# Kernel optimization log

Hardware: AMD Instinct MI355X
Metric: run time of the kernel (lower is better)

The kernel has to match this reference:

```python
import jax, jax.numpy as jnp
import numpy as np

N_NODES = 100000
IN_CH, HID_CH, OUT_CH = 128, 256, 128
N_EDGES = 1600000


def setup_inputs() -> dict:
    key = jax.random.key(0)
    k_x, k_e, k_w1, k_b1, k_w2, k_b2 = jax.random.split(key, 6)
    x = jax.random.normal(k_x, (N_NODES, IN_CH), dtype=jnp.float32)
    edge_index = jax.random.randint(k_e, (2, N_EDGES), 0, N_NODES, dtype=jnp.int64)
    # MLP params (Linear stores weight [out,in]; we keep [in,out] for x @ W)
    lim1 = 1.0 / np.sqrt(IN_CH)
    lim2 = 1.0 / np.sqrt(HID_CH)
    W1 = jax.random.uniform(k_w1, (IN_CH, HID_CH), jnp.float32, -lim1, lim1)
    b1 = jax.random.uniform(k_b1, (HID_CH,), jnp.float32, -lim1, lim1)
    W2 = jax.random.uniform(k_w2, (HID_CH, OUT_CH), jnp.float32, -lim2, lim2)
    b2 = jax.random.uniform(k_b2, (OUT_CH,), jnp.float32, -lim2, lim2)
    eps = jnp.zeros((), jnp.float32)  # train_eps=True, init 0
    return {"x": x, "edge_index": edge_index, "W1": W1, "b1": b1,
            "W2": W2, "b2": b2, "eps": eps}


def reference(x, edge_index, W1, b1, W2, b2, eps):
    src, dst = edge_index[0], edge_index[1]
    # scatter-add neighbor aggregation: aggr[i] = sum_{(j->i)} x[j]
    aggr = jax.ops.segment_sum(x[src], dst, num_segments=N_NODES)  # [N, in]
    h = (1.0 + eps) * x + aggr
    h = jax.nn.relu(h @ W1 + b1)
    h = h @ W2 + b2
    h = jax.nn.relu(h)
    # dropout is identity in eval mode
    return jax.nn.log_softmax(h, axis=-1)
```

## Files before the change

### kernel.cpp

```cpp
#include <hip/hip_runtime.h>

#define N_NODES 100000
#define IN_CH 128
#define HID_CH 256
#define OUT_CH 128
#define N_EDGES 1600000

#define NBK 782
#define BIN_BLOCKS 256
#define EPB (N_EDGES / BIN_BLOCKS)
#define BKT_CAP 4096

typedef __attribute__((ext_vector_type(8))) short short8;
typedef __attribute__((ext_vector_type(4))) float f32x4;

__device__ __forceinline__ float b2f(ushort u) {
    unsigned int x = ((unsigned int)u) << 16;
    return __uint_as_float(x);
}
__device__ __forceinline__ ushort f2b(float f) {
    unsigned int u = __float_as_uint(f);
    u += 0x7FFFu + ((u >> 16) & 1u);
    return (ushort)(u >> 16);
}

#define PREP_X_BLOCKS 6250
#define PREP_W1_BLOCKS 128
#define PREP_W2_BLOCKS 128
#define PREP_TOTAL (PREP_X_BLOCKS + PREP_W1_BLOCKS + PREP_W2_BLOCKS)
__global__ __launch_bounds__(256) void prep_kernel(
    const float* __restrict__ x, const float* __restrict__ W1,
    const float* __restrict__ W2, const int* __restrict__ dst,
    ushort* __restrict__ xb, ushort* __restrict__ W1T,
    ushort* __restrict__ W2T, int* __restrict__ histT) {
    const int b = blockIdx.x;
    const int t = threadIdx.x;
    if (b < PREP_X_BLOCKS) {
        const size_t i = (size_t)b * 2048 + t * 8;
        float4 a = *reinterpret_cast<const float4*>(x + i);
        float4 c = *reinterpret_cast<const float4*>(x + i + 4);
        ushort v[8] = {f2b(a.x), f2b(a.y), f2b(a.z), f2b(a.w),
                       f2b(c.x), f2b(c.y), f2b(c.z), f2b(c.w)};
        *reinterpret_cast<short8*>(xb + i) = *reinterpret_cast<short8*>(v);
    } else if (b < PREP_X_BLOCKS + PREP_W1_BLOCKS) {
        const int i = (b - PREP_X_BLOCKS) * 256 + t;
        const int oc = i >> 7, k = i & 127;
        W1T[i] = f2b(W1[k * HID_CH + oc]);
    } else if (b < PREP_TOTAL) {
        const int i = (b - PREP_X_BLOCKS - PREP_W1_BLOCKS) * 256 + t;
        const int oc = i >> 8, k = i & 255;
        W2T[i] = f2b(W2[k * OUT_CH + oc]);
    } else {
        __shared__ int h[NBK];
        const int bb = b - PREP_TOTAL;
        for (int k = t; k < NBK; k += 256) h[k] = 0;
        __syncthreads();
        const int base = bb * EPB;
        for (int i = t; i < EPB; i += 256)
            atomicAdd(&h[dst[base + i] >> 7], 1);
        __syncthreads();
        for (int k = t; k < NBK; k += 256) histT[k * BIN_BLOCKS + bb] = h[k];
    }
}

__global__ __launch_bounds__(256) void scanA_kernel(
    const int* __restrict__ histT, int* __restrict__ blockBaseP,
    int* __restrict__ bktTotal) {
    __shared__ int ts[256];
    const int bk = blockIdx.x, t = threadIdx.x;
    const int v = histT[bk * BIN_BLOCKS + t];
    ts[t] = v;
    __syncthreads();
    #pragma unroll
    for (int o = 1; o < 256; o <<= 1) {
        int add = (t >= o) ? ts[t - o] : 0;
        __syncthreads();
        ts[t] += add;
        __syncthreads();
    }
    blockBaseP[bk * BIN_BLOCKS + t] = ts[t] - v;
    if (t == 255) bktTotal[bk] = ts[255];
}

__global__ __launch_bounds__(256) void bin_kernel(
    const int* __restrict__ src, const int* __restrict__ dst,
    const int* __restrict__ blockBaseP,
    unsigned int* __restrict__ ebuf) {
    __shared__ int base[NBK];
    __shared__ int cur[NBK];
    const int b = blockIdx.x, t = threadIdx.x;
    for (int k = t; k < NBK; k += 256) {
        base[k] = k * BKT_CAP + blockBaseP[k * BIN_BLOCKS + b];
        cur[k] = 0;
    }
    __syncthreads();
    const int ebase = b * EPB;
    for (int i = t; i < EPB; i += 256) {
        const int d = dst[ebase + i];
        const int s = src[ebase + i];
        const int bk = d >> 7;
        const int r = atomicAdd(&cur[bk], 1);
        ebuf[base[bk] + r] = ((unsigned int)(d & 127) << 17) | (unsigned int)s;
    }
}

__global__ __launch_bounds__(256) void group_kernel(
    const unsigned int* __restrict__ ebuf,
    const int* __restrict__ bktTotal,
    int* __restrict__ csr_src, int* __restrict__ begA, int* __restrict__ endA) {
    __shared__ int hist[128];
    __shared__ int cur[128];
    const int bk = blockIdx.x, t = threadIdx.x;
    if (t < 128) hist[t] = 0;
    __syncthreads();
    const int start = bk * BKT_CAP;
    const int cnt   = bktTotal[bk];
    for (int i = t; i < cnt; i += 256)
        atomicAdd(&hist[ebuf[start + i] >> 17], 1);
    __syncthreads();
    int v = (t < 128) ? hist[t] : 0;
    #pragma unroll
    for (int o = 1; o < 128; o <<= 1) {
        int add = (t < 128 && t >= o) ? hist[t - o] : 0;
        __syncthreads();
        if (t < 128) hist[t] += add;
        __syncthreads();
    }
    if (t < 128) {
        const int excl = hist[t] - v;
        cur[t] = excl;
        const int node = bk * 128 + t;
        if (node < N_NODES) {
            begA[node] = start + excl;
            endA[node] = start + hist[t];
        }
    }
    __syncthreads();
    for (int i = t; i < cnt; i += 256) {
        const unsigned int e = ebuf[start + i];
        const int dl = e >> 17;
        const int p = atomicAdd(&cur[dl], 1);
        csr_src[start + p] = (int)(e & 0x1FFFF);
    }
}

__global__ __launch_bounds__(256) void gather_kernel(
    const ushort* __restrict__ xb,
    const float* __restrict__ eps_p,
    const int* __restrict__ begA,
    const int* __restrict__ endA,
    const int* __restrict__ csr_src,
    ushort* __restrict__ h_in) {
    const int node = blockIdx.x * 8 + (threadIdx.x >> 5);
    const int l32 = threadIdx.x & 31;
    const int c = l32 * 4;
    const int beg = begA[node];
    const int end = endA[node];

    float4 A0 = {0.f,0.f,0.f,0.f}, A1 = {0.f,0.f,0.f,0.f};
    float4 A2 = {0.f,0.f,0.f,0.f}, A3 = {0.f,0.f,0.f,0.f};

    for (int base = beg; base < end; base += 32) {
        const int nn = min(32, end - base);
        const int sidx = csr_src[base + min(l32, nn - 1)];
        int i = 0;
        for (; i + 4 <= nn; i += 4) {
            const int s0 = __shfl(sidx, i + 0, 32);
            const int s1 = __shfl(sidx, i + 1, 32);
            const int s2 = __shfl(sidx, i + 2, 32);
            const int s3 = __shfl(sidx, i + 3, 32);
            ushort4 v0 = *reinterpret_cast<const ushort4*>(xb + (size_t)s0 * IN_CH + c);
            ushort4 v1 = *reinterpret_cast<const ushort4*>(xb + (size_t)s1 * IN_CH + c);
            ushort4 v2 = *reinterpret_cast<const ushort4*>(xb + (size_t)s2 * IN_CH + c);
            ushort4 v3 = *reinterpret_cast<const ushort4*>(xb + (size_t)s3 * IN_CH + c);
            A0.x += b2f(v0.x); A0.y += b2f(v0.y); A0.z += b2f(v0.z); A0.w += b2f(v0.w);
            A1.x += b2f(v1.x); A1.y += b2f(v1.y); A1.z += b2f(v1.z); A1.w += b2f(v1.w);
            A2.x += b2f(v2.x); A2.y += b2f(v2.y); A2.z += b2f(v2.z); A2.w += b2f(v2.w);
            A3.x += b2f(v3.x); A3.y += b2f(v3.y); A3.z += b2f(v3.z); A3.w += b2f(v3.w);
        }
        for (; i < nn; ++i) {
            const int s = __shfl(sidx, i, 32);
            ushort4 v = *reinterpret_cast<const ushort4*>(xb + (size_t)s * IN_CH + c);
            A0.x += b2f(v.x); A0.y += b2f(v.y); A0.z += b2f(v.z); A0.w += b2f(v.w);
        }
    }

    const float a0 = A0.x + A1.x + A2.x + A3.x;
    const float a1 = A0.y + A1.y + A2.y + A3.y;
    const float a2 = A0.z + A1.z + A2.z + A3.z;
    const float a3 = A0.w + A1.w + A2.w + A3.w;

    const float scale = 1.0f + eps_p[0];
    ushort4 sv = *reinterpret_cast<const ushort4*>(xb + (size_t)node * IN_CH + c);
    ushort4 o;
    o.x = f2b(scale * b2f(sv.x) + a0);
    o.y = f2b(scale * b2f(sv.y) + a1);
    o.z = f2b(scale * b2f(sv.z) + a2);
    o.w = f2b(scale * b2f(sv.w) + a3);
    *reinterpret_cast<ushort4*>(h_in + (size_t)node * IN_CH + c) = o;
}

__global__ __launch_bounds__(512, 4) void mlp_fused(
    const ushort* __restrict__ h_in,
    const ushort* __restrict__ W1T,
    const ushort* __restrict__ W2T,
    const float* __restrict__ b1,
    const float* __restrict__ b2,
    float* __restrict__ out) {
    __shared__ ushort wbuf[32768];
    const int t    = threadIdx.x;
    const int w    = t >> 6;
    const int lane = t & 63;
    const int lr   = lane & 15;
    const int lk   = lane >> 4;
    const int row0 = blockIdx.x * 128 + w * 16;
    const int arow = row0 + lr;
    const int arc  = arow < N_NODES ? arow : N_NODES - 1;
    const int sw = (lr & 7) << 3;

    {
        const ushort* gw = W1T + t * 64;
        const int row = t >> 1;
        const int s = (row & 7) << 3;
        ushort* dstp = wbuf + row * 128;
        #pragma unroll
        for (int j = 0; j < 8; ++j) {
            short8 v = *reinterpret_cast<const short8*>(gw + j * 8);
            const int col = (t & 1) * 64 + j * 8;
            *reinterpret_cast<short8*>(dstp + (col ^ s)) = v;
        }
    }

    short8 a[4];
    const ushort* ap = h_in + (size_t)arc * IN_CH + lk * 8;
    #pragma unroll
    for (int kk = 0; kk < 4; ++kk)
        a[kk] = *reinterpret_cast<const short8*>(ap + kk * 32);

    __syncthreads();

    int pk[16][2];
    #pragma unroll
    for (int ct = 0; ct < 16; ++ct) {
        const ushort* bp = wbuf + (ct * 16 + lr) * 128;
        f32x4 acc = (f32x4){0.f, 0.f, 0.f, 0.f};
        #pragma unroll
        for (int kk = 0; kk < 4; ++kk) {
            short8 wf = *reinterpret_cast<const short8*>(bp + ((lk * 8 + kk * 32) ^ sw));
            acc = __builtin_amdgcn_mfma_f32_16x16x32_bf16(wf, a[kk], acc, 0, 0, 0);
        }
        const float4 bb = *reinterpret_cast<const float4*>(b1 + ct * 16 + lk * 4);
        const float v0 = fmaxf(acc[0] + bb.x, 0.0f);
        const float v1 = fmaxf(acc[1] + bb.y, 0.0f);
        const float v2 = fmaxf(acc[2] + bb.z, 0.0f);
        const float v3 = fmaxf(acc[3] + bb.w, 0.0f);
        pk[ct][0] = (int)f2b(v0) | ((int)f2b(v1) << 16);
        pk[ct][1] = (int)f2b(v2) | ((int)f2b(v3) << 16);
    }

    __syncthreads();

    {
        const ushort* gw = W2T + t * 64;
        const int row = t >> 2;
        const int s = (row & 7) << 3;
        ushort* dstp = wbuf + row * 256;
        #pragma unroll
        for (int j = 0; j < 8; ++j) {
            short8 v = *reinterpret_cast<const short8*>(gw + j * 8);
            const int col = (t & 3) * 64 + j * 8;
            *reinterpret_cast<short8*>(dstp + (col ^ s)) = v;
        }
    }

    short8 a2[8];
    #pragma unroll
    for (int kk2 = 0; kk2 < 8; ++kk2) {
        const int lo0 = pk[2 * kk2][0],     lo1 = pk[2 * kk2][1];
        const int hi0 = pk[2 * kk2 + 1][0], hi1 = pk[2 * kk2 + 1][1];
        union { int d[4]; short8 s8; } u;
        #pragma unroll
        for (int i = 0; i < 4; ++i) {
            const int srcLane = lr + 16 * ((2 * lk + (i >> 1)) & 3);
            const int vlo = __shfl((i & 1) ? lo1 : lo0, srcLane, 64);
            const int vhi = __shfl((i & 1) ? hi1 : hi0, srcLane, 64);
            u.d[i] = (lk < 2) ? vlo : vhi;
        }
        a2[kk2] = u.s8;
    }

    __syncthreads();

    f32x4 acc2[8];
    #pragma unroll
    for (int ct = 0; ct < 8; ++ct) acc2[ct] = (f32x4){0.f, 0.f, 0.f, 0.f};

    #pragma unroll
    for (int ct = 0; ct < 8; ++ct) {
        const ushort* bp = wbuf + (ct * 16 + lr) * 256;
        #pragma unroll
        for (int kk = 0; kk < 8; ++kk) {
            short8 b = *reinterpret_cast<const short8*>(bp + ((lk * 8 + kk * 32) ^ sw));
            acc2[ct] = __builtin_amdgcn_mfma_f32_16x16x32_bf16(a2[kk], b, acc2[ct], 0, 0, 0);
        }
    }

    float bias[8];
    #pragma unroll
    for (int ct = 0; ct < 8; ++ct) bias[ct] = b2[ct * 16 + lr];

    const int orow0 = row0 + lk * 4;
    #pragma unroll
    for (int r = 0; r < 4; ++r) {
        float v[8];
        float m = -1e30f;
        #pragma unroll
        for (int ct = 0; ct < 8; ++ct) {
            v[ct] = fmaxf(acc2[ct][r] + bias[ct], 0.0f);
            m = fmaxf(m, v[ct]);
        }
        #pragma unroll
        for (int o = 1; o < 16; o <<= 1) m = fmaxf(m, __shfl_xor(m, o));
        float s = 0.0f;
        #pragma unroll
        for (int ct = 0; ct < 8; ++ct) s += __expf(v[ct] - m);
        #pragma unroll
        for (int o = 1; o < 16; o <<= 1) s += __shfl_xor(s, o);
        const float lse = m + __logf(s);
        const int orow = orow0 + r;
        if (orow < N_NODES) {
            #pragma unroll
            for (int ct = 0; ct < 8; ++ct)
                out[(size_t)orow * OUT_CH + ct * 16 + lr] = v[ct] - lse;
        }
    }
}

extern "C" void kernel_launch(void* const* d_in, const int* in_sizes, int n_in,
                              void* d_out, int out_size, void* d_ws, size_t ws_size,
                              hipStream_t stream) {
    const float* x    = (const float*)d_in[0];
    const int*   ei   = (const int*)d_in[1];
    const float* W1   = (const float*)d_in[2];
    const float* b1   = (const float*)d_in[3];
    const float* W2   = (const float*)d_in[4];
    const float* b2   = (const float*)d_in[5];
    const float* eps  = (const float*)d_in[6];
    float* out = (float*)d_out;

    ushort* xb   = (ushort*)d_ws;
    ushort* h_in = xb + (size_t)N_NODES * IN_CH;
    ushort* W1T  = h_in + (size_t)N_NODES * IN_CH;
    ushort* W2T  = W1T + IN_CH * HID_CH;
    int* histT      = (int*)(W2T + HID_CH * OUT_CH);
    int* blockBaseP = histT + NBK * BIN_BLOCKS;
    int* bktTotal   = blockBaseP + NBK * BIN_BLOCKS;
    int* begA       = bktTotal + NBK;
    int* endA       = begA + N_NODES;
    unsigned int* ebuf = (unsigned int*)(endA + N_NODES);
    int* csr_src    = (int*)(ebuf + (size_t)NBK * BKT_CAP);

    const int* src = ei;
    const int* dst = ei + N_EDGES;

    prep_kernel<<<PREP_TOTAL + BIN_BLOCKS, 256, 0, stream>>>(
        x, W1, W2, dst, xb, W1T, W2T, histT);
    scanA_kernel<<<NBK, 256, 0, stream>>>(histT, blockBaseP, bktTotal);
    bin_kernel<<<BIN_BLOCKS, 256, 0, stream>>>(src, dst, blockBaseP, ebuf);
    group_kernel<<<NBK, 256, 0, stream>>>(ebuf, bktTotal, csr_src, begA, endA);
    gather_kernel<<<N_NODES / 8, 256, 0, stream>>>(xb, eps, begA, endA, csr_src, h_in);
    mlp_fused<<<(N_NODES + 127) / 128, 512, 0, stream>>>(h_in, W1T, W2T, b1, b2, out);
}
```

Before: 159.3 us.

## Stage bucket scatter in shared memory and widen gather unroll

The bin kernel now builds a local histogram and prefix sum, sorts its edges by bucket in shared memory, then copies each bucket segment contiguously to global memory instead of scattering single words. The group kernel caches its bucket in shared memory and writes csr_src as one coalesced pass after a shared-memory sort. The gather loop unrolls to 8 independent accumulators to keep more loads in flight. The cost is an extra read of dst and higher shared memory and register use. The per-thread serial copy loops in bin_kernel are poorly coalesced, and clamping cnt to BKT_CAP silently drops edges if a bucket overflows.

```diff
diff --git a/kernel.cpp b/kernel.cpp
--- a/kernel.cpp
+++ b/kernel.cpp
@@ -86,21 +86,56 @@
     const int* __restrict__ src, const int* __restrict__ dst,
     const int* __restrict__ blockBaseP,
     unsigned int* __restrict__ ebuf) {
-    __shared__ int base[NBK];
+    __shared__ unsigned int srt[EPB];
+    __shared__ int h[NBK];
     __shared__ int cur[NBK];
+    __shared__ int part[256];
     const int b = blockIdx.x, t = threadIdx.x;
-    for (int k = t; k < NBK; k += 256) {
-        base[k] = k * BKT_CAP + blockBaseP[k * BIN_BLOCKS + b];
-        cur[k] = 0;
-    }
+    for (int k = t; k < NBK; k += 256) h[k] = 0;
     __syncthreads();
     const int ebase = b * EPB;
+    for (int i = t; i < EPB; i += 256)
+        atomicAdd(&h[dst[ebase + i] >> 7], 1);
+    __syncthreads();
+    const int k0 = t * 4;
+    const int s0 = (k0 + 0 < NBK) ? h[k0 + 0] : 0;
+    const int s1 = (k0 + 1 < NBK) ? h[k0 + 1] : 0;
+    const int s2 = (k0 + 2 < NBK) ? h[k0 + 2] : 0;
+    const int s3 = (k0 + 3 < NBK) ? h[k0 + 3] : 0;
+    const int tot = s0 + s1 + s2 + s3;
+    part[t] = tot;
+    __syncthreads();
+    #pragma unroll
+    for (int o = 1; o < 256; o <<= 1) {
+        int add = (t >= o) ? part[t - o] : 0;
+        __syncthreads();
+        part[t] += add;
+        __syncthreads();
+    }
+    const int excl = part[t] - tot;
+    if (k0 + 0 < NBK) { h[k0 + 0] = excl;               cur[k0 + 0] = excl; }
+    if (k0 + 1 < NBK) { h[k0 + 1] = excl + s0;          cur[k0 + 1] = excl + s0; }
+    if (k0 + 2 < NBK) { h[k0 + 2] = excl + s0 + s1;     cur[k0 + 2] = excl + s0 + s1; }
+    if (k0 + 3 < NBK) { h[k0 + 3] = excl + s0 + s1 + s2; cur[k0 + 3] = excl + s0 + s1 + s2; }
+    __syncthreads();
     for (int i = t; i < EPB; i += 256) {
         const int d = dst[ebase + i];
         const int s = src[ebase + i];
         const int bk = d >> 7;
-        const int r = atomicAdd(&cur[bk], 1);
-        ebuf[base[bk] + r] = ((unsigned int)(d & 127) << 17) | (unsigned int)s;
+        const int p = atomicAdd(&cur[bk], 1);
+        srt[p] = ((unsigned int)(d & 127) << 17) | (unsigned int)s;
+    }
+    __syncthreads();
+    #pragma unroll
+    for (int j = 0; j < 4; ++j) {
+        const int k = k0 + j;
+        if (k < NBK) {
+            const int lb = h[k];
+            const int le = cur[k];
+            unsigned int* gp = ebuf + (size_t)k * BKT_CAP
+                             + blockBaseP[k * BIN_BLOCKS + b];
+            for (int p = lb; p < le; ++p) gp[p - lb] = srt[p];
+        }
     }
 }
 
@@ -108,15 +143,20 @@
     const unsigned int* __restrict__ ebuf,
     const int* __restrict__ bktTotal,
     int* __restrict__ csr_src, int* __restrict__ begA, int* __restrict__ endA) {
+    __shared__ unsigned int ein[BKT_CAP];
+    __shared__ int srt[BKT_CAP];
     __shared__ int hist[128];
     __shared__ int cur[128];
     const int bk = blockIdx.x, t = threadIdx.x;
     if (t < 128) hist[t] = 0;
     __syncthreads();
     const int start = bk * BKT_CAP;
-    const int cnt   = bktTotal[bk];
-    for (int i = t; i < cnt; i += 256)
-        atomicAdd(&hist[ebuf[start + i] >> 17], 1);
+    const int cnt = min(bktTotal[bk], BKT_CAP);
+    for (int i = t; i < cnt; i += 256) {
+        const unsigned int e = ebuf[start + i];
+        ein[i] = e;
+        atomicAdd(&hist[e >> 17], 1);
+    }
     __syncthreads();
     int v = (t < 128) ? hist[t] : 0;
     #pragma unroll
@@ -137,11 +177,14 @@
     }
     __syncthreads();
     for (int i = t; i < cnt; i += 256) {
-        const unsigned int e = ebuf[start + i];
+        const unsigned int e = ein[i];
         const int dl = e >> 17;
         const int p = atomicAdd(&cur[dl], 1);
-        csr_src[start + p] = (int)(e & 0x1FFFF);
-    }
+        srt[p] = (int)(e & 0x1FFFF);
+    }
+    __syncthreads();
+    for (int i = t; i < cnt; i += 256)
+        csr_src[start + i] = srt[i];
 }
 
 __global__ __launch_bounds__(256) void gather_kernel(
@@ -159,24 +202,38 @@
 
     float4 A0 = {0.f,0.f,0.f,0.f}, A1 = {0.f,0.f,0.f,0.f};
     float4 A2 = {0.f,0.f,0.f,0.f}, A3 = {0.f,0.f,0.f,0.f};
+    float4 A4 = {0.f,0.f,0.f,0.f}, A5 = {0.f,0.f,0.f,0.f};
+    float4 A6 = {0.f,0.f,0.f,0.f}, A7 = {0.f,0.f,0.f,0.f};
 
     for (int base = beg; base < end; base += 32) {
         const int nn = min(32, end - base);
         const int sidx = csr_src[base + min(l32, nn - 1)];
         int i = 0;
-        for (; i + 4 <= nn; i += 4) {
+        for (; i + 8 <= nn; i += 8) {
             const int s0 = __shfl(sidx, i + 0, 32);
             const int s1 = __shfl(sidx, i + 1, 32);
             const int s2 = __shfl(sidx, i + 2, 32);
             const int s3 = __shfl(sidx, i + 3, 32);
+            const int s4 = __shfl(sidx, i + 4, 32);
+            const int s5 = __shfl(sidx, i + 5, 32);
+            const int s6 = __shfl(sidx, i + 6, 32);
+            const int s7 = __shfl(sidx, i + 7, 32);
             ushort4 v0 = *reinterpret_cast<const ushort4*>(xb + (size_t)s0 * IN_CH + c);
             ushort4 v1 = *reinterpret_cast<const ushort4*>(xb + (size_t)s1 * IN_CH + c);
             ushort4 v2 = *reinterpret_cast<const ushort4*>(xb + (size_t)s2 * IN_CH + c);
             ushort4 v3 = *reinterpret_cast<const ushort4*>(xb + (size_t)s3 * IN_CH + c);
+            ushort4 v4 = *reinterpret_cast<const ushort4*>(xb + (size_t)s4 * IN_CH + c);
+            ushort4 v5 = *reinterpret_cast<const ushort4*>(xb + (size_t)s5 * IN_CH + c);
+            ushort4 v6 = *reinterpret_cast<const ushort4*>(xb + (size_t)s6 * IN_CH + c);
+            ushort4 v7 = *reinterpret_cast<const ushort4*>(xb + (size_t)s7 * IN_CH + c);
             A0.x += b2f(v0.x); A0.y += b2f(v0.y); A0.z += b2f(v0.z); A0.w += b2f(v0.w);
             A1.x += b2f(v1.x); A1.y += b2f(v1.y); A1.z += b2f(v1.z); A1.w += b2f(v1.w);
             A2.x += b2f(v2.x); A2.y += b2f(v2.y); A2.z += b2f(v2.z); A2.w += b2f(v2.w);
             A3.x += b2f(v3.x); A3.y += b2f(v3.y); A3.z += b2f(v3.z); A3.w += b2f(v3.w);
+            A4.x += b2f(v4.x); A4.y += b2f(v4.y); A4.z += b2f(v4.z); A4.w += b2f(v4.w);
+            A5.x += b2f(v5.x); A5.y += b2f(v5.y); A5.z += b2f(v5.z); A5.w += b2f(v5.w);
+            A6.x += b2f(v6.x); A6.y += b2f(v6.y); A6.z += b2f(v6.z); A6.w += b2f(v6.w);
+            A7.x += b2f(v7.x); A7.y += b2f(v7.y); A7.z += b2f(v7.z); A7.w += b2f(v7.w);
         }
         for (; i < nn; ++i) {
             const int s = __shfl(sidx, i, 32);
@@ -185,10 +242,10 @@
         }
     }
 
-    const float a0 = A0.x + A1.x + A2.x + A3.x;
-    const float a1 = A0.y + A1.y + A2.y + A3.y;
-    const float a2 = A0.z + A1.z + A2.z + A3.z;
-    const float a3 = A0.w + A1.w + A2.w + A3.w;
+    const float a0 = ((A0.x + A1.x) + (A2.x + A3.x)) + ((A4.x + A5.x) + (A6.x + A7.x));
+    const float a1 = ((A0.y + A1.y) + (A2.y + A3.y)) + ((A4.y + A5.y) + (A6.y + A7.y));
+    const float a2 = ((A0.z + A1.z) + (A2.z + A3.z)) + ((A4.z + A5.z) + (A6.z + A7.z));
+    const float a3 = ((A0.w + A1.w) + (A2.w + A3.w)) + ((A4.w + A5.w) + (A6.w + A7.w));
 
     const float scale = 1.0f + eps_p[0];
     ushort4 sv = *reinterpret_cast<const ushort4*>(xb + (size_t)node * IN_CH + c);
```

Result: slower. 170.7 us (+7.2%).
